# Optimization experiments

Hardware: AMD Instinct MI355X
Metric: run time of the kernel (lower is better)

The kernel has to match this reference:

```python
import jax, jax.numpy as jnp
import numpy as np

H = W = 1024          # image_shape (square)
ZP, PH, PW = 16, 32, 32   # psf z-stack shape
THRESH = 2.0          # detection_threshold
K = 1024              # spots_per_frame
ROISIZE = PW          # default roisize = psf.shape[-1]
BG_R = PW * 2         # default bg_filter_size
MAXF = PW             # default max_filter_size


def setup_inputs() -> dict:
    key = jax.random.key(0)
    k1, k2 = jax.random.split(key)
    image = jax.random.uniform(k1, (H, W), jnp.float32) * 100.0
    psf = jax.random.uniform(k2, (ZP, PH, PW), jnp.float32)
    psf = psf / jnp.sum(psf, axis=(1, 2), keepdims=True)  # normalized PSF stack
    return {"image": image, "psf": psf}


def _precompute_filters(psf):
    pad = (H - PH) // 2  # square image/psf -> same pad both dims
    psf_padded = jnp.pad(psf, ((0, 0), (pad, pad), (pad, pad)))
    psf_padded = jnp.fft.fftshift(psf_padded, axes=(1, 2))
    psf_fd = jnp.flip(jnp.fft.fft2(psf_padded), axis=(1, 2))
    rr = (jnp.arange(H) - H // 2)[:, None] ** 2 + (jnp.arange(W) - W // 2)[None, :] ** 2
    bg = (rr < BG_R ** 2).astype(jnp.float32) / (np.pi * BG_R ** 2)
    bg_fd = jnp.fft.fft2(jnp.fft.fftshift(bg))
    return psf_fd, bg_fd


def reference(image, psf):
    psf_fd, bg_fd = _precompute_filters(psf)
    image_fd = jnp.fft.fft2(image)
    conv_psf = jnp.fft.ifft2(image_fd[None] * psf_fd).real       # [Z,H,W]
    conv_bg = jnp.fft.ifft2(image_fd * bg_fd).real               # [H,W]
    ratio = conv_psf / (conv_bg[None] + 1.0)                     # matched-filter SNR
    result = ratio.max(axis=0)                                   # [H,W]
    zmap = jnp.argmax(ratio, axis=0)                             # best z plane

    # MaxPool2d(MAXF, stride=1, padding=MAXF//2-1): torch pads with -inf,
    # output is [H-1,W-1]; torch code then zero-pads one row/col at top-left.
    p = MAXF // 2 - 1
    mx = jax.lax.reduce_window(result, -jnp.inf, jax.lax.max,
                               (MAXF, MAXF), (1, 1), ((p, p), (p, p)))
    mx = jnp.pad(mx, ((1, 0), (1, 0)))                           # back to [H,W]

    mask = jnp.where((mx == result) & (result > THRESH), result, 0.0)
    values, indices = jax.lax.top_k(mask.ravel(), K)
    x = indices % W
    y = indices // H  # torch divides by input_shape[0]; square so == W
    roy = y - ROISIZE // 2
    rox = x - ROISIZE // 2
    valid = ((values > THRESH)
             & (roy >= 0) & (roy < H - ROISIZE)
             & (rox >= 0) & (rox < W - ROISIZE))

    # fixed-shape version of boolean select: clamp for safe gather, mask invalids
    roy_c = jnp.clip(roy, 0, H - ROISIZE)
    rox_c = jnp.clip(rox, 0, W - ROISIZE)
    r = jnp.arange(ROISIZE)
    Y = roy_c[:, None, None] + r[None, :, None]                  # [K,R,1]
    X = rox_c[:, None, None] + r[None, None, :]                  # [K,1,R]
    rois = image[Y, X] * valid[:, None, None].astype(image.dtype)  # [K,R,R]

    roipos = jnp.stack((roy_c, rox_c), -1) * valid[:, None]
    intensity = values * valid
    return roipos, intensity, rois, valid
```

## Files before the change

### kernel.cpp

```cpp
#include <hip/hip_runtime.h>
#include <stdint.h>

typedef float v4f __attribute__((ext_vector_type(4)));
typedef float f2u __attribute__((ext_vector_type(2), aligned(4)));
typedef unsigned long long ull2 __attribute__((ext_vector_type(2), aligned(8)));

#define PEX_STRIDE 1156
#define WS_IMG8   0
#define WS_BFRAG  1048576
#define WS_PEX    1064960
#define WS_RB     5799936
#define WS_RESULT 9994240
#define WS_CAND   14188544

__device__ inline unsigned char f32_to_e4m3(float v) {
    if (!(v > 0.0f)) return 0;
    if (v >= 448.0f) return 0x7e;
    if (v < 0.015625f) {
        int m = (int)(v * 512.0f + 0.5f);
        if (m > 7) return 0x08;
        return (unsigned char)m;
    }
    unsigned int u = __float_as_uint(v) + 0x00080000u;
    int e = (int)((u >> 23) & 0xff) - 127;
    int m3 = (int)(u >> 20) & 7;
    int e8 = e + 7;
    if (e8 >= 16) return 0x7e;
    return (unsigned char)((e8 << 3) | m3);
}

__global__ void k_zb(const float* __restrict__ psf, unsigned char* __restrict__ bf,
                     unsigned int* cnt, float4* __restrict__ out, int n4) {
    int blk = blockIdx.x;
    if (blk < 1056) {
        int i = blk * 256 + threadIdx.x;
        if (i < n4) { float4 z; z.x = z.y = z.z = z.w = 0.f; out[i] = z; }
    } else {
        int t = (blk - 1056) * 256 + threadIdx.x;
        if (t == 0) cnt[0] = 0u;
        int kb = t >> 9; int l = (t >> 3) & 63; int j = t & 7;
        int z = l & 15; int q = l >> 4;
        int a = kb; int b = q * 8 + j;
        float p = psf[z * 1024 + a * 32 + b];
        float c = cosf((float)(a + b - 32) * (6.283185307179586f / 1024.0f));
        bf[kb * 512 + l * 8 + j] = f32_to_e4m3(p * c * 1024.0f);
    }
}

__global__ void k_pex(const float* __restrict__ img, float* __restrict__ pex,
                      uint32_t* __restrict__ img8) {
    __shared__ float wtot[4];
    int r = blockIdx.x, t = threadIdx.x;
    const float* row = img + r * 1024;
    float s[5];
    float acc = 0.f;
    int base = t * 5;
    #pragma unroll
    for (int j = 0; j < 5; j++) {
        int c = base + j;
        float v = (c < 1152) ? row[(c - 64) & 1023] : 0.f;
        acc += v; s[j] = acc;
    }
    float sc = acc;
    int lane = t & 63, w = t >> 6;
    #pragma unroll
    for (int off = 1; off < 64; off <<= 1) {
        float v = __shfl_up(sc, off, 64);
        if (lane >= off) sc += v;
    }
    if (lane == 63) wtot[w] = sc;
    __syncthreads();
    float wbase = 0.f;
    #pragma unroll
    for (int i = 0; i < 3; i++) if (i < w) wbase += wtot[i];
    float excl = wbase + (sc - acc);
    float* prow = pex + r * PEX_STRIDE;
    if (t == 0) prow[0] = 0.f;
    #pragma unroll
    for (int j = 0; j < 5; j++) {
        int c = base + j;
        if (c < 1152) prow[c + 1] = excl + s[j];
    }
    float4 v4 = *(const float4*)(row + 4 * t);
    img8[r * 256 + t] = (uint32_t)f32_to_e4m3(v4.x)
                      | ((uint32_t)f32_to_e4m3(v4.y) << 8)
                      | ((uint32_t)f32_to_e4m3(v4.z) << 16)
                      | ((uint32_t)f32_to_e4m3(v4.w) << 24);
}

__global__ __launch_bounds__(256) void k_bg(const float* __restrict__ pex,
                                            float* __restrict__ rb) {
    static constexpr int W[64] = {
        63,63,63,63,63,63,63,63,63,63,63,63,
        62,62,62,62, 61,61,61,61, 60,60,60, 59,59, 58,58,58, 57,57, 56,
        55,55, 54,54, 53, 52,52, 51, 50, 49,49,
        48,47,46,45,44,43,42,41,
        39,38,37,35,34,32,30,29,27,24,22,19,15,11
    };
    int blk = blockIdx.x;
    int xcd = blk & 7;
    int sub = blk >> 4;
    int half = (blk >> 3) & 1;
    int s = xcd * 16 + sub;
    int row = s * 8 + 3;
    int n0 = (half << 9) + ((int)threadIdx.x << 1);
    f2u acc0, acc1;
    {
        const float* pr = pex + row * PEX_STRIDE + n0;
        acc0 = *(const f2u*)(pr + 128) - *(const f2u*)(pr + 1);
        acc1 = (f2u)0.f;
    }
    #pragma unroll 3
    for (int dy = 1; dy <= 63; dy++) {
        const int w = W[dy];
        const float* p1 = pex + ((row - dy) & 1023) * PEX_STRIDE + n0;
        const float* p2 = pex + ((row + dy) & 1023) * PEX_STRIDE + n0;
        acc0 += *(const f2u*)(p1 + 65 + w) - *(const f2u*)(p1 + 64 - w);
        acc1 += *(const f2u*)(p2 + 65 + w) - *(const f2u*)(p2 + 64 - w);
    }
    f2u sum = acc0 + acc1;
    const float k = (float)(1.0 / (3.14159265358979323846 * 4096.0));
    f2u r2;
    r2.x = 1.0f / ((sum.x * k + 1.0f) * 1024.0f);
    r2.y = 1.0f / ((sum.y * k + 1.0f) * 1024.0f);
    *(f2u*)(rb + s * 1024 + n0) = r2;
}

__global__ __launch_bounds__(512, 2) void k_conv(
    const unsigned long long* __restrict__ img64,
    const unsigned long long* __restrict__ bfrag,
    const float* __restrict__ rb, float* __restrict__ result) {
    __shared__ unsigned long long sm[7936];
    int tid = threadIdx.x;
    int wave = tid >> 6, lane = tid & 63;
    int b = blockIdx.x;
    int tr = b >> 5, tc = b & 31;
    int r0 = tr * 64, c0 = tc * 32;

    for (int u = tid; u < 665; u += 512) {
        int dr = u / 7;
        int x8 = u - dr * 7;
        int row = (r0 + dr - 16) & 1023;
        int cb0 = (c0 + x8 * 8 - 16) & 1023;
        int cb1 = (cb0 + 8) & 1023;
        unsigned long long lo = img64[row * 128 + (cb0 >> 3)];
        unsigned long long hi = img64[row * 128 + (cb1 >> 3)];
        int dst = dr * 9 + x8;
        sm[dst] = lo;
        #pragma unroll
        for (int s = 1; s < 8; s++)
            sm[s * 856 + dst] = (lo >> (8 * s)) | (hi << (64 - 8 * s));
    }
    __syncthreads();

    int i0 = (wave >> 1) * 16;
    int cw = (wave & 1) * 16;
    int q = lane >> 4;
    int lane_off = (lane & 15) * 9 + q;

    v4f acc[16];
    #pragma unroll
    for (int f = 0; f < 16; f++) acc[f] = (v4f)0.0f;

    unsigned long long bnext = bfrag[lane];
    int rowbase = i0 * 9 + lane_off + (cw >> 3);
    for (int kb = 0; kb < 32; kb++) {
        unsigned long long bcur = bnext;
        bnext = bfrag[((kb < 31 ? kb + 1 : 31) << 6) + lane];
        int abase = rowbase + kb * 9;
        #pragma unroll
        for (int cc = 0; cc < 8; cc++) {
            ull2 a2 = *(const ull2*)(sm + abase + cc * 856);
            acc[cc]     = __builtin_amdgcn_mfma_f32_16x16x32_fp8_fp8(
                (long)a2.x, (long)bcur, acc[cc], 0, 0, 0);
            acc[cc + 8] = __builtin_amdgcn_mfma_f32_16x16x32_fp8_fp8(
                (long)a2.y, (long)bcur, acc[cc + 8], 0, 0, 0);
        }
    }

    float* epi = (float*)(sm + 6848) + wave * 272;
    #pragma unroll
    for (int cc = 0; cc < 16; cc++) {
        v4f v = acc[cc];
        #pragma unroll
        for (int m = 1; m < 16; m <<= 1) {
            v.x = fmaxf(v.x, __shfl_xor(v.x, m, 64));
            v.y = fmaxf(v.y, __shfl_xor(v.y, m, 64));
            v.z = fmaxf(v.z, __shfl_xor(v.z, m, 64));
            v.w = fmaxf(v.w, __shfl_xor(v.w, m, 64));
        }
        if ((lane & 15) == cc) {
            epi[(q * 4 + 0) * 17 + cc] = v.x;
            epi[(q * 4 + 1) * 17 + cc] = v.y;
            epi[(q * 4 + 2) * 17 + cc] = v.z;
            epi[(q * 4 + 3) * 17 + cc] = v.w;
        }
    }
    __syncthreads();
    #pragma unroll
    for (int rr = 0; rr < 4; rr++) {
        int prow = q * 4 + rr;
        int grow = r0 + i0 + prow;
        int gcol = c0 + cw + (lane & 15);
        result[grow * 1024 + gcol] =
            epi[prow * 17 + (lane & 15)] * rb[(grow >> 3) * 1024 + gcol];
    }
}

__global__ __launch_bounds__(256) void k_maxcand(const float* __restrict__ result,
                                                 unsigned int* cnt,
                                                 unsigned long long* cand) {
    __shared__ float ls[95 * 96];
    __shared__ float hr[95 * 64];
    __shared__ float wmax[4];
    int bx = blockIdx.x & 15, by = blockIdx.x >> 4;
    int i0 = by * 64, j0 = bx * 64;
    int t = threadIdx.x;
    const float* cb = result + i0 * 1024 + j0;
    float mx = -3.4e38f;
    #pragma unroll
    for (int k = 0; k < 16; k++) {
        int idx = k * 256 + t;
        mx = fmaxf(mx, cb[(idx >> 6) * 1024 + (idx & 63)]);
    }
    #pragma unroll
    for (int m = 1; m < 64; m <<= 1) mx = fmaxf(mx, __shfl_xor(mx, m, 64));
    if ((t & 63) == 0) wmax[t >> 6] = mx;
    __syncthreads();
    float tmax = fmaxf(fmaxf(wmax[0], wmax[1]), fmaxf(wmax[2], wmax[3]));
    if (tmax <= 2.0f) return;

    for (int idx = t; idx < 95 * 95; idx += 256) {
        int r = idx / 95, c = idx - r * 95;
        int gr = i0 - 16 + r, gc = j0 - 16 + c;
        float v = -3.4e38f;
        if ((unsigned)gr < 1024u && (unsigned)gc < 1024u) v = result[gr * 1024 + gc];
        ls[r * 96 + c] = v;
    }
    __syncthreads();
    for (int idx = t; idx < 95 * 64; idx += 256) {
        int r = idx >> 6, c = idx & 63;
        const float* p = ls + r * 96 + c;
        float m = p[0];
        #pragma unroll
        for (int d = 1; d < 32; d++) m = fmaxf(m, p[d]);
        hr[idx] = m;
    }
    __syncthreads();
    for (int idx = t; idx < 64 * 64; idx += 256) {
        int r = idx >> 6, c = idx & 63;
        const float* p = hr + r * 64 + c;
        float m = p[0];
        #pragma unroll
        for (int d = 1; d < 32; d++) m = fmaxf(m, p[d * 64]);
        float v = ls[(r + 16) * 96 + (c + 16)];
        int gi = i0 + r, gj = j0 + c;
        if (gi >= 1 && gj >= 1 && v > 2.0f && v == m) {
            unsigned int k = atomicAdd(cnt, 1u);
            if (k < 2048)
                cand[k] = ((unsigned long long)__float_as_uint(v) << 32)
                        | (unsigned int)(~(unsigned int)(gi * 1024 + gj));
        }
    }
}

__global__ __launch_bounds__(1024) void k_final(
    const float* __restrict__ image, const unsigned int* __restrict__ cnt,
    const unsigned long long* __restrict__ cand, float* __restrict__ out) {
    __shared__ unsigned long long keys[2048];
    int t = threadIdx.x;
    int n = (int)cnt[0]; if (n > 2048) n = 2048;
    if (n == 0) return;
    for (int k = t; k < 2048; k += 1024) keys[k] = (k < n) ? cand[k] : 0ull;
    __syncthreads();
    for (int size = 2; size <= 2048; size <<= 1) {
        for (int stride = size >> 1; stride > 0; stride >>= 1) {
            for (int i = t; i < 2048; i += 1024) {
                int ixj = i ^ stride;
                if (ixj > i) {
                    unsigned long long a = keys[i], b = keys[ixj];
                    bool sw = ((i & size) == 0) ? (a < b) : (a > b);
                    if (sw) { keys[i] = b; keys[ixj] = a; }
                }
            }
            __syncthreads();
        }
    }
    float* roipos = out;
    float* intensity = out + 2048;
    float* rois = out + 3072;
    float* validf = out + 3072 + 1048576;
    int nw = n < 1024 ? n : 1024;
    if (t < nw) {
        unsigned long long key = keys[t];
        float val = __uint_as_float((unsigned int)(key >> 32));
        unsigned int p = ~(unsigned int)key;
        int y = (int)(p >> 10), x = (int)(p & 1023);
        int roy = y - 16, rox = x - 16;
        bool valid = (roy >= 0 && roy < 992 && rox >= 0 && rox < 992);
        int royc = roy < 0 ? 0 : (roy > 992 ? 992 : roy);
        int roxc = rox < 0 ? 0 : (rox > 992 ? 992 : rox);
        roipos[2 * t]     = valid ? (float)royc : 0.f;
        roipos[2 * t + 1] = valid ? (float)roxc : 0.f;
        intensity[t]      = valid ? val : 0.f;
        validf[t]         = valid ? 1.f : 0.f;
    }
    __syncthreads();
    for (int k = 0; k < nw; k++) {
        unsigned long long key = keys[k];
        unsigned int p = ~(unsigned int)key;
        int y = (int)(p >> 10), x = (int)(p & 1023);
        int roy = y - 16, rox = x - 16;
        if (!(roy >= 0 && roy < 992 && rox >= 0 && rox < 992)) continue;
        int u = t >> 5, vv = t & 31;
        rois[k * 1024 + t] = image[(roy + u) * 1024 + (rox + vv)];
    }
}

extern "C" void kernel_launch(void* const* d_in, const int* in_sizes, int n_in,
                              void* d_out, int out_size, void* d_ws, size_t ws_size,
                              hipStream_t stream) {
    const float* image = (const float*)d_in[0];
    const float* psf   = (const float*)d_in[1];
    float* out = (float*)d_out;
    char* ws = (char*)d_ws;
    unsigned char* img8  = (unsigned char*)(ws + WS_IMG8);
    unsigned char* bfrag = (unsigned char*)(ws + WS_BFRAG);
    float* pex = (float*)(ws + WS_PEX);
    float* rb  = (float*)(ws + WS_RB);
    float* result = (float*)(ws + WS_RESULT);
    unsigned int* cnt = (unsigned int*)(ws + WS_CAND);
    unsigned long long* cand = (unsigned long long*)(ws + WS_CAND + 16);

    int n4 = out_size / 4;
    hipLaunchKernelGGL(k_zb,      dim3(1120), dim3(256), 0, stream,
                       psf, bfrag, cnt, (float4*)d_out, n4);
    hipLaunchKernelGGL(k_pex,     dim3(1024), dim3(256), 0, stream, image, pex, (uint32_t*)img8);
    hipLaunchKernelGGL(k_bg,      dim3(256),  dim3(256), 0, stream, pex, rb);
    hipLaunchKernelGGL(k_conv,    dim3(512),  dim3(512), 0, stream,
                       (const unsigned long long*)img8, (const unsigned long long*)bfrag, rb, result);
    hipLaunchKernelGGL(k_maxcand, dim3(256),  dim3(256), 0, stream, result, cnt, cand);
    hipLaunchKernelGGL(k_final,   dim3(1),    dim3(1024), 0, stream, image, cnt, cand, out);
}
```

Baseline: 118.7 us.

## Swap MFMA operand roles in conv, shuffle-only epilogue, merge setup kernels

Merges the zeroing and PSF-fragment setup kernel into k_pex as extra blocks, removing one launch. In k_conv the PSF fragment becomes the A operand, so z-planes land in the row dimension and image pixels in the column dimension. This lets the max over z be done with in-register maxes plus two cross-lane shuffles, replacing the LDS-staged epilogue and its barrier. The LDS shift-plane stride changes to 858 to alter bank mapping, and k_maxcand's block-max prescan uses float4 loads. The risk is a correctness error in the transposed fragment indexing, plus LDS reads that are now scalar 64-bit instead of 128-bit.

```diff
diff --git a/kernel.cpp b/kernel.cpp
--- a/kernel.cpp
+++ b/kernel.cpp
@@ -3,9 +3,9 @@
 
 typedef float v4f __attribute__((ext_vector_type(4)));
 typedef float f2u __attribute__((ext_vector_type(2), aligned(4)));
-typedef unsigned long long ull2 __attribute__((ext_vector_type(2), aligned(8)));
 
 #define PEX_STRIDE 1156
+#define CSTRIDE 858
 #define WS_IMG8   0
 #define WS_BFRAG  1048576
 #define WS_PEX    1064960
@@ -29,28 +29,29 @@
     return (unsigned char)((e8 << 3) | m3);
 }
 
-__global__ void k_zb(const float* __restrict__ psf, unsigned char* __restrict__ bf,
-                     unsigned int* cnt, float4* __restrict__ out, int n4) {
-    int blk = blockIdx.x;
-    if (blk < 1056) {
-        int i = blk * 256 + threadIdx.x;
-        if (i < n4) { float4 z; z.x = z.y = z.z = z.w = 0.f; out[i] = z; }
-    } else {
-        int t = (blk - 1056) * 256 + threadIdx.x;
-        if (t == 0) cnt[0] = 0u;
-        int kb = t >> 9; int l = (t >> 3) & 63; int j = t & 7;
-        int z = l & 15; int q = l >> 4;
-        int a = kb; int b = q * 8 + j;
-        float p = psf[z * 1024 + a * 32 + b];
-        float c = cosf((float)(a + b - 32) * (6.283185307179586f / 1024.0f));
-        bf[kb * 512 + l * 8 + j] = f32_to_e4m3(p * c * 1024.0f);
-    }
-}
-
 __global__ void k_pex(const float* __restrict__ img, float* __restrict__ pex,
-                      uint32_t* __restrict__ img8) {
+                      uint32_t* __restrict__ img8, const float* __restrict__ psf,
+                      unsigned char* __restrict__ bf, unsigned int* cnt,
+                      float4* __restrict__ out, int n4) {
     __shared__ float wtot[4];
-    int r = blockIdx.x, t = threadIdx.x;
+    int blk = blockIdx.x, t = threadIdx.x;
+    if (blk >= 1024) {
+        if (blk < 2080) {
+            int i = (blk - 1024) * 256 + t;
+            if (i < n4) { float4 z; z.x = z.y = z.z = z.w = 0.f; out[i] = z; }
+        } else {
+            int u = (blk - 2080) * 256 + t;
+            if (u == 0) cnt[0] = 0u;
+            int kb = u >> 9; int l = (u >> 3) & 63; int j = u & 7;
+            int z = l & 15; int q = l >> 4;
+            int a = kb; int b = q * 8 + j;
+            float p = psf[z * 1024 + a * 32 + b];
+            float c = cosf((float)(a + b - 32) * (6.283185307179586f / 1024.0f));
+            bf[kb * 512 + l * 8 + j] = f32_to_e4m3(p * c * 1024.0f);
+        }
+        return;
+    }
+    int r = blk;
     const float* row = img + r * 1024;
     float s[5];
     float acc = 0.f;
@@ -130,7 +131,7 @@
     const unsigned long long* __restrict__ img64,
     const unsigned long long* __restrict__ bfrag,
     const float* __restrict__ rb, float* __restrict__ result) {
-    __shared__ unsigned long long sm[7936];
+    __shared__ unsigned long long sm[8 * CSTRIDE];
     int tid = threadIdx.x;
     int wave = tid >> 6, lane = tid & 63;
     int b = blockIdx.x;
@@ -149,61 +150,53 @@
         sm[dst] = lo;
         #pragma unroll
         for (int s = 1; s < 8; s++)
-            sm[s * 856 + dst] = (lo >> (8 * s)) | (hi << (64 - 8 * s));
+            sm[s * CSTRIDE + dst] = (lo >> (8 * s)) | (hi << (64 - 8 * s));
     }
     __syncthreads();
 
     int i0 = (wave >> 1) * 16;
     int cw = (wave & 1) * 16;
-    int q = lane >> 4;
-    int lane_off = (lane & 15) * 9 + q;
+    int g = lane >> 4;
+    int slot = ((cw + (lane & 15)) >> 3) + g;
+    const unsigned long long* bp = sm + (lane & 7) * CSTRIDE + slot + i0 * 9;
 
     v4f acc[16];
     #pragma unroll
     for (int f = 0; f < 16; f++) acc[f] = (v4f)0.0f;
 
-    unsigned long long bnext = bfrag[lane];
-    int rowbase = i0 * 9 + lane_off + (cw >> 3);
+    unsigned long long anext = bfrag[lane];
     for (int kb = 0; kb < 32; kb++) {
-        unsigned long long bcur = bnext;
-        bnext = bfrag[((kb < 31 ? kb + 1 : 31) << 6) + lane];
-        int abase = rowbase + kb * 9;
+        unsigned long long acur = anext;
+        anext = bfrag[((kb < 31 ? kb + 1 : 31) << 6) + lane];
+        const unsigned long long* pk = bp + kb * 9;
         #pragma unroll
-        for (int cc = 0; cc < 8; cc++) {
-            ull2 a2 = *(const ull2*)(sm + abase + cc * 856);
+        for (int cc = 0; cc < 16; cc += 2) {
+            unsigned long long b0 = pk[cc * 9];
+            unsigned long long b1 = pk[cc * 9 + 9];
             acc[cc]     = __builtin_amdgcn_mfma_f32_16x16x32_fp8_fp8(
-                (long)a2.x, (long)bcur, acc[cc], 0, 0, 0);
-            acc[cc + 8] = __builtin_amdgcn_mfma_f32_16x16x32_fp8_fp8(
-                (long)a2.y, (long)bcur, acc[cc + 8], 0, 0, 0);
+                (long)acur, (long)b0, acc[cc], 0, 0, 0);
+            acc[cc + 1] = __builtin_amdgcn_mfma_f32_16x16x32_fp8_fp8(
+                (long)acur, (long)b1, acc[cc + 1], 0, 0, 0);
         }
     }
 
-    float* epi = (float*)(sm + 6848) + wave * 272;
+    float zmax[16];
     #pragma unroll
     for (int cc = 0; cc < 16; cc++) {
         v4f v = acc[cc];
-        #pragma unroll
-        for (int m = 1; m < 16; m <<= 1) {
-            v.x = fmaxf(v.x, __shfl_xor(v.x, m, 64));
-            v.y = fmaxf(v.y, __shfl_xor(v.y, m, 64));
-            v.z = fmaxf(v.z, __shfl_xor(v.z, m, 64));
-            v.w = fmaxf(v.w, __shfl_xor(v.w, m, 64));
-        }
-        if ((lane & 15) == cc) {
-            epi[(q * 4 + 0) * 17 + cc] = v.x;
-            epi[(q * 4 + 1) * 17 + cc] = v.y;
-            epi[(q * 4 + 2) * 17 + cc] = v.z;
-            epi[(q * 4 + 3) * 17 + cc] = v.w;
-        }
-    }
-    __syncthreads();
-    #pragma unroll
-    for (int rr = 0; rr < 4; rr++) {
-        int prow = q * 4 + rr;
-        int grow = r0 + i0 + prow;
-        int gcol = c0 + cw + (lane & 15);
-        result[grow * 1024 + gcol] =
-            epi[prow * 17 + (lane & 15)] * rb[(grow >> 3) * 1024 + gcol];
+        float m = fmaxf(fmaxf(v.x, v.y), fmaxf(v.z, v.w));
+        m = fmaxf(m, __shfl_xor(m, 16, 64));
+        m = fmaxf(m, __shfl_xor(m, 32, 64));
+        zmax[cc] = m;
+    }
+    int gcol = c0 + cw + (lane & 15);
+    #pragma unroll
+    for (int c4 = 0; c4 < 4; c4++) {
+        float m01 = (g & 1) ? zmax[c4 * 4 + 1] : zmax[c4 * 4 + 0];
+        float m23 = (g & 1) ? zmax[c4 * 4 + 3] : zmax[c4 * 4 + 2];
+        float m = (g & 2) ? m23 : m01;
+        int grow = r0 + i0 + c4 * 4 + g;
+        result[grow * 1024 + gcol] = m * rb[(grow >> 3) * 1024 + gcol];
     }
 }
 
@@ -216,12 +209,13 @@
     int bx = blockIdx.x & 15, by = blockIdx.x >> 4;
     int i0 = by * 64, j0 = bx * 64;
     int t = threadIdx.x;
-    const float* cb = result + i0 * 1024 + j0;
+    const float4* cb4 = (const float4*)(result + i0 * 1024 + j0);
     float mx = -3.4e38f;
     #pragma unroll
-    for (int k = 0; k < 16; k++) {
+    for (int k = 0; k < 4; k++) {
         int idx = k * 256 + t;
-        mx = fmaxf(mx, cb[(idx >> 6) * 1024 + (idx & 63)]);
+        float4 v = cb4[(idx >> 4) * 256 + (idx & 15)];
+        mx = fmaxf(mx, fmaxf(fmaxf(v.x, v.y), fmaxf(v.z, v.w)));
     }
     #pragma unroll
     for (int m = 1; m < 64; m <<= 1) mx = fmaxf(mx, __shfl_xor(mx, m, 64));
@@ -333,9 +327,8 @@
     unsigned long long* cand = (unsigned long long*)(ws + WS_CAND + 16);
 
     int n4 = out_size / 4;
-    hipLaunchKernelGGL(k_zb,      dim3(1120), dim3(256), 0, stream,
-                       psf, bfrag, cnt, (float4*)d_out, n4);
-    hipLaunchKernelGGL(k_pex,     dim3(1024), dim3(256), 0, stream, image, pex, (uint32_t*)img8);
+    hipLaunchKernelGGL(k_pex,     dim3(2144), dim3(256), 0, stream,
+                       image, pex, (uint32_t*)img8, psf, bfrag, cnt, (float4*)d_out, n4);
     hipLaunchKernelGGL(k_bg,      dim3(256),  dim3(256), 0, stream, pex, rb);
     hipLaunchKernelGGL(k_conv,    dim3(512),  dim3(512), 0, stream,
                        (const unsigned long long*)img8, (const unsigned long long*)bfrag, rb, result);
```

Result: faster. 102.6 us (-13.6%).
